# Kernel tuning notes

Measured on AMD Instinct MI355X. Metric: run time of the kernel, lower is better.

Reference implementation:

```python
import jax, jax.numpy as jnp
import numpy as np
import math


def setup_inputs() -> dict:
    key = jax.random.key(0)
    ks = jax.random.split(key, 16)
    B, S, H, K, PREV = 32, 2048, 1024, 4, 2
    sc = 0.02
    return {
        "last_hidden": jax.random.normal(ks[0], (1, B, H), jnp.float32),
        "decoder_inputs": jax.random.normal(ks[1], (B, 1, H), jnp.float32),
        "encoder_outputs": jax.random.normal(ks[2], (B, S, H), jnp.float32),
        "attention_scores": jax.random.normal(ks[3], (PREV, B, 1, S), jnp.float32),
        "attention_mask": jnp.zeros((B, 1, S), jnp.float32),
        "evidence_scores": jax.random.uniform(ks[4], (B,), jnp.float32),
        "evidence_sentence_index": jax.random.randint(ks[5], (B, PREV), 0, S, dtype=jnp.int32),
        "W_ih": jax.random.normal(ks[6], (3 * H, H), jnp.float32) * sc,
        "W_hh": jax.random.normal(ks[7], (3 * H, H), jnp.float32) * sc,
        "b_ih": jax.random.normal(ks[8], (3 * H,), jnp.float32) * sc,
        "b_hh": jax.random.normal(ks[9], (3 * H,), jnp.float32) * sc,
        "Wk": jax.random.normal(ks[10], (H, H), jnp.float32) * sc,
        "bk": jnp.zeros((H,), jnp.float32),
        "Wv": jax.random.normal(ks[11], (H, H), jnp.float32) * sc,
        "bv": jnp.zeros((H,), jnp.float32),
        "topk": K,
    }


def _gru_step(x, h, W_ih, W_hh, b_ih, b_hh):
    # x, h: (B, H). PyTorch GRU cell math.
    gi = x @ W_ih.T + b_ih  # (B, 3H)
    gh = h @ W_hh.T + b_hh  # (B, 3H)
    i_r, i_z, i_n = jnp.split(gi, 3, axis=1)
    h_r, h_z, h_n = jnp.split(gh, 3, axis=1)
    r = jax.nn.sigmoid(i_r + h_r)
    z = jax.nn.sigmoid(i_z + h_z)
    n = jnp.tanh(i_n + r * h_n)
    return (1.0 - z) * n + z * h


def reference(last_hidden, decoder_inputs, encoder_outputs, attention_scores,
              attention_mask, evidence_scores, evidence_sentence_index,
              W_ih, W_hh, b_ih, b_hh, Wk, bk, Wv, bv, topk):
    B, S, H = encoder_outputs.shape
    K = topk
    R = B // K  # real batch (beam groups)

    key_eo = encoder_outputs @ Wk.T + bk    # (B, S, H)
    val_eo = encoder_outputs @ Wv.T + bv    # (B, S, H)

    h_new = _gru_step(decoder_inputs[:, 0], last_hidden[0], W_ih, W_hh, b_ih, b_hh)  # (B, H)
    output = h_new[:, None, :]              # (B, 1, H)

    attn_outputs = jnp.einsum('bih,bsh->bis', output, key_eo) / math.sqrt(H) + attention_mask  # (B,1,S)
    attn_alignment = jax.nn.softmax(attn_outputs, axis=-1)
    context = jnp.einsum('bis,bsh->bih', attn_alignment, val_eo)  # (B, 1, H)

    # top-k per beam, then joint rerank over topk*topk candidates per real example
    vals, idx = jax.lax.top_k(attn_alignment.reshape(R, K, S), K)  # (R, K, K), sorted desc
    scores = vals.reshape(B, K)
    sentences = idx.reshape(B, K)
    log_scores = -jnp.log(scores) + evidence_scores[:, None]       # (B, K)

    flat = log_scores.reshape(R, K * K)
    order = jnp.argsort(flat, axis=-1)[:, :K]                      # (R, K) ascending, stable
    new_evidence_scores = jnp.take_along_axis(flat, order, axis=1).reshape(B)
    s_flat = (order // K + jnp.arange(R)[:, None] * K).reshape(B)  # source beam in [0, B)
    r_flat = (order % K).reshape(B)

    sel_sent = sentences[s_flat, r_flat]                           # (B,)
    result = context[s_flat]                                       # (B, 1, H)
    hidden = h_new[s_flat][None]                                   # (1, B, H)
    new_evidence_sentence_index = jnp.concatenate(
        [evidence_sentence_index[s_flat], sel_sent[:, None].astype(evidence_sentence_index.dtype)], axis=1)
    new_attention_scores = jnp.concatenate(
        [attention_scores[:, s_flat], attn_outputs[s_flat][None]], axis=0)  # (prev+1, B, 1, S)
    new_attention_mask = attention_mask[s_flat]                    # (B, 1, S)

    return (result, hidden, new_evidence_sentence_index,
            new_attention_scores, new_attention_mask, new_evidence_scores)
```

## Files before the change

### kernel.cpp

```cpp
#include <hip/hip_runtime.h>
#include <hip/hip_bf16.h>
#include <cfloat>
#include <climits>
#include <cmath>

#define BB 32
#define SS 2048
#define HH 1024
#define KK 4
#define CH 32

__global__ __launch_bounds__(256) void gates_partial(
    const float* __restrict__ x, const float* __restrict__ h_old,
    const float* __restrict__ W_ih, const float* __restrict__ W_hh,
    float* __restrict__ part) {
  int t = threadIdx.x;
  int jb = blockIdx.x;
  int k0 = blockIdx.y * 64;
  bool second = (jb >= 12);
  const float* A = second ? h_old : x;
  const float* W = second ? W_hh : W_ih;
  int j0 = jb * 256;
  int jr = j0 - (second ? 3072 : 0);
  const float* wp = W + (size_t)(jr + t) * HH + k0;
  float acc[32];
#pragma unroll
  for (int b = 0; b < 32; b++) acc[b] = 0.f;
  for (int kk = 0; kk < 64; kk += 4) {
    float4 wv = *(const float4*)(wp + kk);
#pragma unroll
    for (int b = 0; b < 32; b++) {
      float4 a = *(const float4*)(A + (size_t)b * HH + k0 + kk);
      acc[b] += a.x * wv.x + a.y * wv.y + a.z * wv.z + a.w * wv.w;
    }
  }
  float* pb = part + (size_t)blockIdx.y * (32 * 6144) + j0 + t;
#pragma unroll
  for (int b = 0; b < 32; b++) pb[(size_t)b * 6144] = acc[b];
}

__global__ __launch_bounds__(256) void gru_q(
    const float* __restrict__ part, const float* __restrict__ b_ih,
    const float* __restrict__ b_hh, const float* __restrict__ h_old,
    const float* __restrict__ Wk, float* __restrict__ h_new,
    float* __restrict__ qpart2) {
  __shared__ float hs[256];
  int t = threadIdx.x;
  int kc = blockIdx.x, b = blockIdx.y, z = blockIdx.z;
  int h = kc * 256 + t;
  float s0 = 0.f, s1 = 0.f, s2 = 0.f, s3 = 0.f, s4 = 0.f, s5 = 0.f;
#pragma unroll
  for (int c = 0; c < 16; c++) {
    const float* p = part + ((size_t)c * 32 + b) * 6144;
    s0 += p[h];
    s1 += p[1024 + h];
    s2 += p[2048 + h];
    s3 += p[3072 + h];
    s4 += p[4096 + h];
    s5 += p[5120 + h];
  }
  float ir = s0 + b_ih[h], iz = s1 + b_ih[1024 + h], in_ = s2 + b_ih[2048 + h];
  float hr = s3 + b_hh[h], hz = s4 + b_hh[1024 + h], hn = s5 + b_hh[2048 + h];
  float r = 1.f / (1.f + expf(-(ir + hr)));
  float z_ = 1.f / (1.f + expf(-(iz + hz)));
  float n = tanhf(in_ + r * hn);
  float hv = (1.f - z_) * n + z_ * h_old[b * HH + h];
  if (z == 0) h_new[b * HH + h] = hv;
  hs[t] = hv;
  __syncthreads();
  float2 acc = make_float2(0.f, 0.f);
  const float* wb = Wk + (size_t)kc * 256 * HH + z * 512 + 2 * t;
  for (int k = 0; k < 256; k += 4) {
    float2 w0 = *(const float2*)(wb + (size_t)(k + 0) * HH);
    float2 w1 = *(const float2*)(wb + (size_t)(k + 1) * HH);
    float2 w2 = *(const float2*)(wb + (size_t)(k + 2) * HH);
    float2 w3 = *(const float2*)(wb + (size_t)(k + 3) * HH);
    float a0 = hs[k], a1 = hs[k + 1], a2 = hs[k + 2], a3 = hs[k + 3];
    acc.x += a0 * w0.x + a1 * w1.x + a2 * w2.x + a3 * w3.x;
    acc.y += a0 * w0.y + a1 * w1.y + a2 * w2.y + a3 * w3.y;
  }
  *(float2*)(qpart2 + ((size_t)b * 4 + kc) * HH + z * 512 + 2 * t) = acc;
}

__global__ __launch_bounds__(256) void fused_attn(
    const float* __restrict__ eo, const float* __restrict__ qpart2,
    const float* __restrict__ h_new, const float* __restrict__ bk,
    const float* __restrict__ mask, float* __restrict__ logits,
    float* __restrict__ c0part, float* __restrict__ msum_part) {
  __shared__ float q_lds[HH];
  __shared__ float wred[4];
  __shared__ float cacc[4][1024];
  __shared__ float cms[4][2];
  int b = blockIdx.y, sc = blockIdx.x, t = threadIdx.x;
  int w = t >> 6, lane = t & 63;
  {
    float4 qs = *(const float4*)(qpart2 + ((size_t)b * 4 + 0) * HH + 4 * t);
#pragma unroll
    for (int kc = 1; kc < 4; kc++) {
      float4 v = *(const float4*)(qpart2 + ((size_t)b * 4 + kc) * HH + 4 * t);
      qs.x += v.x; qs.y += v.y; qs.z += v.z; qs.w += v.w;
    }
    *(float4*)&q_lds[4 * t] = qs;
    float4 hv = *(const float4*)(h_new + (size_t)b * HH + 4 * t);
    float4 kv = *(const float4*)(bk + 4 * t);
    float p = hv.x * kv.x + hv.y * kv.y + hv.z * kv.z + hv.w * kv.w;
#pragma unroll
    for (int off = 32; off; off >>= 1) p += __shfl_xor(p, off);
    if (lane == 0) wred[w] = p;
  }
  __syncthreads();
  float hb = wred[0] + wred[1] + wred[2] + wred[3];
  float4 qv[4];
#pragma unroll
  for (int i = 0; i < 4; i++) qv[i] = *(const float4*)&q_lds[(i * 64 + lane) * 4];

  float m = -FLT_MAX, sum = 0.f;
  float4 acc[4];
#pragma unroll
  for (int i = 0; i < 4; i++) acc[i] = make_float4(0.f, 0.f, 0.f, 0.f);
  int rbase = sc * 64 + w * 16;
  for (int tile = 0; tile < 8; tile++) {
    int r0 = rbase + tile * 2;
    float4 rv[2][4];
#pragma unroll
    for (int rr = 0; rr < 2; rr++) {
      const float4* e4 = (const float4*)(eo + ((size_t)b * SS + r0 + rr) * HH);
#pragma unroll
      for (int i = 0; i < 4; i++) rv[rr][i] = e4[i * 64 + lane];
    }
    float p0 = 0.f, p1 = 0.f;
#pragma unroll
    for (int i = 0; i < 4; i++) {
      p0 += rv[0][i].x * qv[i].x + rv[0][i].y * qv[i].y +
            rv[0][i].z * qv[i].z + rv[0][i].w * qv[i].w;
      p1 += rv[1][i].x * qv[i].x + rv[1][i].y * qv[i].y +
            rv[1][i].z * qv[i].z + rv[1][i].w * qv[i].w;
    }
#pragma unroll
    for (int off = 32; off; off >>= 1) {
      p0 += __shfl_xor(p0, off);
      p1 += __shfl_xor(p1, off);
    }
    float lv0 = (p0 + hb) * 0.03125f + mask[(size_t)b * SS + r0];
    float lv1 = (p1 + hb) * 0.03125f + mask[(size_t)b * SS + r0 + 1];
    if (lane == 0) {
      logits[(size_t)b * SS + r0] = lv0;
      logits[(size_t)b * SS + r0 + 1] = lv1;
    }
    float m_new = fmaxf(m, fmaxf(lv0, lv1));
    float scale = expf(m - m_new);
    float w0 = expf(lv0 - m_new), w1 = expf(lv1 - m_new);
    sum = sum * scale + w0 + w1;
#pragma unroll
    for (int i = 0; i < 4; i++) {
      acc[i].x = acc[i].x * scale + w0 * rv[0][i].x + w1 * rv[1][i].x;
      acc[i].y = acc[i].y * scale + w0 * rv[0][i].y + w1 * rv[1][i].y;
      acc[i].z = acc[i].z * scale + w0 * rv[0][i].z + w1 * rv[1][i].z;
      acc[i].w = acc[i].w * scale + w0 * rv[0][i].w + w1 * rv[1][i].w;
    }
    m = m_new;
  }
#pragma unroll
  for (int i = 0; i < 4; i++) *(float4*)&cacc[w][i * 256 + lane * 4] = acc[i];
  if (lane == 0) { cms[w][0] = m; cms[w][1] = sum; }
  __syncthreads();
  float m0 = cms[0][0], m1 = cms[1][0], m2 = cms[2][0], m3 = cms[3][0];
  float mb = fmaxf(fmaxf(m0, m1), fmaxf(m2, m3));
  float wt0 = expf(m0 - mb), wt1 = expf(m1 - mb), wt2 = expf(m2 - mb),
        wt3 = expf(m3 - mb);
  float sb = cms[0][1] * wt0 + cms[1][1] * wt1 + cms[2][1] * wt2 + cms[3][1] * wt3;
  float4 a0 = *(float4*)&cacc[0][4 * t];
  float4 a1 = *(float4*)&cacc[1][4 * t];
  float4 a2 = *(float4*)&cacc[2][4 * t];
  float4 a3 = *(float4*)&cacc[3][4 * t];
  float4 r;
  r.x = wt0 * a0.x + wt1 * a1.x + wt2 * a2.x + wt3 * a3.x;
  r.y = wt0 * a0.y + wt1 * a1.y + wt2 * a2.y + wt3 * a3.y;
  r.z = wt0 * a0.z + wt1 * a1.z + wt2 * a2.z + wt3 * a3.z;
  r.w = wt0 * a0.w + wt1 * a1.w + wt2 * a2.w + wt3 * a3.w;
  *(float4*)(c0part + ((size_t)sc * 32 + b) * 1024 + 4 * t) = r;
  if (t == 0) {
    msum_part[((size_t)sc * 32 + b) * 2 + 0] = mb;
    msum_part[((size_t)sc * 32 + b) * 2 + 1] = sb;
  }
}

__device__ __forceinline__ bool vi_better(float av, int ai, float bv, int bi) {
  return av > bv || (av == bv && ai < bi);
}

__global__ __launch_bounds__(256) void attn_finish(
    const float* __restrict__ c0part, const float* __restrict__ msum_part,
    const float* __restrict__ logits, float* __restrict__ c0,
    float* __restrict__ scores, int* __restrict__ sent) {
  int bid = blockIdx.x, t = threadIdx.x;
  int b = (bid < 128) ? (bid >> 2) : (bid - 128);
  float m = -FLT_MAX;
  float ms[CH];
#pragma unroll
  for (int c = 0; c < CH; c++) {
    ms[c] = msum_part[((size_t)c * 32 + b) * 2 + 0];
    m = fmaxf(m, ms[c]);
  }
  float sum = 0.f;
  float wc[CH];
#pragma unroll
  for (int c = 0; c < CH; c++) {
    wc[c] = expf(ms[c] - m);
    sum += msum_part[((size_t)c * 32 + b) * 2 + 1] * wc[c];
  }
  float inv = 1.f / sum;

  if (bid < 128) {
    int h = (bid & 3) * 256 + t;
    float a = 0.f;
#pragma unroll
    for (int c = 0; c < CH; c++)
      a += wc[c] * c0part[((size_t)c * 32 + b) * 1024 + h];
    c0[(size_t)b * HH + h] = a * inv;
    return;
  }

  float tv0 = -FLT_MAX, tv1 = -FLT_MAX, tv2 = -FLT_MAX, tv3 = -FLT_MAX;
  int ti0 = INT_MAX, ti1 = INT_MAX, ti2 = INT_MAX, ti3 = INT_MAX;
#pragma unroll
  for (int it = 0; it < 8; it++) {
    int idx = it * 256 + t;
    float v = logits[(size_t)b * SS + idx];
    if (vi_better(v, idx, tv3, ti3)) {
      tv3 = v; ti3 = idx;
      if (vi_better(tv3, ti3, tv2, ti2)) { float fv = tv2; int fi = ti2; tv2 = tv3; ti2 = ti3; tv3 = fv; ti3 = fi; }
      if (vi_better(tv2, ti2, tv1, ti1)) { float fv = tv1; int fi = ti1; tv1 = tv2; ti1 = ti2; tv2 = fv; ti2 = fi; }
      if (vi_better(tv1, ti1, tv0, ti0)) { float fv = tv0; int fi = ti0; tv0 = tv1; ti0 = ti1; tv1 = fv; ti1 = fi; }
    }
  }
  __shared__ float sv[256][4];
  __shared__ int si[256][4];
  sv[t][0] = tv0; sv[t][1] = tv1; sv[t][2] = tv2; sv[t][3] = tv3;
  si[t][0] = ti0; si[t][1] = ti1; si[t][2] = ti2; si[t][3] = ti3;
  __syncthreads();
  for (int off = 128; off; off >>= 1) {
    if (t < off) {
      float bv0 = sv[t + off][0], bv1 = sv[t + off][1], bv2 = sv[t + off][2], bv3 = sv[t + off][3];
      int bi0 = si[t + off][0], bi1 = si[t + off][1], bi2 = si[t + off][2], bi3 = si[t + off][3];
      float mv0, mv1, mv2, mv3; int mi0, mi1, mi2, mi3;
      if (vi_better(tv0, ti0, bv3, bi3)) { mv0 = tv0; mi0 = ti0; } else { mv0 = bv3; mi0 = bi3; }
      if (vi_better(tv1, ti1, bv2, bi2)) { mv1 = tv1; mi1 = ti1; } else { mv1 = bv2; mi1 = bi2; }
      if (vi_better(tv2, ti2, bv1, bi1)) { mv2 = tv2; mi2 = ti2; } else { mv2 = bv1; mi2 = bi1; }
      if (vi_better(tv3, ti3, bv0, bi0)) { mv3 = tv3; mi3 = ti3; } else { mv3 = bv0; mi3 = bi0; }
      if (!vi_better(mv0, mi0, mv2, mi2)) { float fv = mv0; int fi = mi0; mv0 = mv2; mi0 = mi2; mv2 = fv; mi2 = fi; }
      if (!vi_better(mv1, mi1, mv3, mi3)) { float fv = mv1; int fi = mi1; mv1 = mv3; mi1 = mi3; mv3 = fv; mi3 = fi; }
      if (!vi_better(mv0, mi0, mv1, mi1)) { float fv = mv0; int fi = mi0; mv0 = mv1; mi0 = mi1; mv1 = fv; mi1 = fi; }
      if (!vi_better(mv2, mi2, mv3, mi3)) { float fv = mv2; int fi = mi2; mv2 = mv3; mi2 = mi3; mv3 = fv; mi3 = fi; }
      tv0 = mv0; tv1 = mv1; tv2 = mv2; tv3 = mv3;
      ti0 = mi0; ti1 = mi1; ti2 = mi2; ti3 = mi3;
      sv[t][0] = tv0; sv[t][1] = tv1; sv[t][2] = tv2; sv[t][3] = tv3;
      si[t][0] = ti0; si[t][1] = ti1; si[t][2] = ti2; si[t][3] = ti3;
    }
    __syncthreads();
  }
  if (t == 0) {
    scores[b * KK + 0] = expf(tv0 - m) * inv; sent[b * KK + 0] = ti0;
    scores[b * KK + 1] = expf(tv1 - m) * inv; sent[b * KK + 1] = ti1;
    scores[b * KK + 2] = expf(tv2 - m) * inv; sent[b * KK + 2] = ti2;
    scores[b * KK + 3] = expf(tv3 - m) * inv; sent[b * KK + 3] = ti3;
  }
}

__global__ __launch_bounds__(256) void ctx_sel_gather(
    const float* __restrict__ scores, const int* __restrict__ sent,
    const float* __restrict__ evidence, const int* __restrict__ esi,
    const float* __restrict__ Wv, const float* __restrict__ bvec,
    const float* __restrict__ c0, const float* __restrict__ hnew,
    const float* __restrict__ attn_in, const float* __restrict__ logits,
    const float* __restrict__ mask, float* __restrict__ out0,
    float* __restrict__ out1, float* __restrict__ out2,
    float* __restrict__ out3, float* __restrict__ out4,
    float* __restrict__ out5) {
  __shared__ int s_sh;
  __shared__ float cs[HH];
  int jq = blockIdx.x, b = blockIdx.y, t = threadIdx.x;
  if (t == 0) {
    int r = b >> 2, j = b & 3;
    float ls[16];
    bool used[16];
    for (int k1 = 0; k1 < 4; k1++)
      for (int k2 = 0; k2 < 4; k2++)
        ls[k1 * 4 + k2] = -logf(scores[(r * 4 + k1) * 4 + k2]) + evidence[r * 4 + k1];
    for (int i = 0; i < 16; i++) used[i] = false;
    int best = 0;
    float bvv = FLT_MAX;
    for (int jj = 0; jj <= j; jj++) {
      best = 0;
      bvv = FLT_MAX;
      for (int i = 0; i < 16; i++)
        if (!used[i] && ls[i] < bvv) { bvv = ls[i]; best = i; }
      used[best] = true;
    }
    int k1 = best >> 2, k2 = best & 3;
    int sSel = r * 4 + k1;
    s_sh = sSel;
    if (jq == 0) {
      out5[b] = bvv;
      out2[b * 3 + 0] = (float)esi[sSel * 2 + 0];
      out2[b * 3 + 1] = (float)esi[sSel * 2 + 1];
      out2[b * 3 + 2] = (float)sent[sSel * 4 + k2];
    }
  }
  __syncthreads();
  int s = s_sh;
  *(float4*)&cs[4 * t] = *(const float4*)(c0 + (size_t)s * HH + 4 * t);
  __syncthreads();
  {
    int j = jq * 256 + t;
    const float4* w4 = (const float4*)(Wv + (size_t)j * HH);
    float acc = bvec[j];
#pragma unroll 8
    for (int k4 = 0; k4 < 256; k4++) {
      float4 wv = w4[k4];
      float4 cc = *(const float4*)&cs[4 * k4];
      acc += wv.x * cc.x + wv.y * cc.y + wv.z * cc.z + wv.w * cc.w;
    }
    out0[(size_t)b * HH + j] = acc;
  }
  out1[(size_t)b * HH + jq * 256 + t] = hnew[(size_t)s * HH + jq * 256 + t];
#pragma unroll
  for (int p = 0; p < 2; p++) {
    *(float2*)(out3 + ((size_t)p * BB + b) * SS + jq * 512 + 2 * t) =
        *(const float2*)(attn_in + ((size_t)p * BB + s) * SS + jq * 512 + 2 * t);
  }
  *(float2*)(out3 + ((size_t)2 * BB + b) * SS + jq * 512 + 2 * t) =
      *(const float2*)(logits + (size_t)s * SS + jq * 512 + 2 * t);
  *(float2*)(out4 + (size_t)b * SS + jq * 512 + 2 * t) =
      *(const float2*)(mask + (size_t)s * SS + jq * 512 + 2 * t);
}

extern "C" void kernel_launch(void* const* d_in, const int* in_sizes, int n_in,
                              void* d_out, int out_size, void* d_ws, size_t ws_size,
                              hipStream_t stream) {
  const float* h_old = (const float*)d_in[0];
  const float* x     = (const float*)d_in[1];
  const float* eo    = (const float*)d_in[2];
  const float* attn_in = (const float*)d_in[3];
  const float* mask  = (const float*)d_in[4];
  const float* evidence = (const float*)d_in[5];
  const int*   esi   = (const int*)d_in[6];
  const float* W_ih  = (const float*)d_in[7];
  const float* W_hh  = (const float*)d_in[8];
  const float* b_ih  = (const float*)d_in[9];
  const float* b_hh  = (const float*)d_in[10];
  const float* Wk    = (const float*)d_in[11];
  const float* bk    = (const float*)d_in[12];
  const float* Wv    = (const float*)d_in[13];
  const float* bv    = (const float*)d_in[14];

  float* w = (float*)d_ws;
  float* h_new  = w + 0;
  float* logits = w + 32768;
  float* scores = w + 98304;
  int*   sent   = (int*)(w + 98432);
  float* c0     = w + 98560;
  float* msum_part = w + 131328;
  float* c0part = w + 133376;
  float* gpart  = w + 1181952;
  float* qpart2 = w + 4327680;

  float* out0 = (float*)d_out;
  float* out1 = out0 + 32768;
  float* out2 = out1 + 32768;
  float* out3 = out2 + 96;
  float* out4 = out3 + 196608;
  float* out5 = out4 + 65536;

  gates_partial<<<dim3(24, 16), 256, 0, stream>>>(x, h_old, W_ih, W_hh, gpart);
  gru_q<<<dim3(4, 32, 2), 256, 0, stream>>>(gpart, b_ih, b_hh, h_old, Wk, h_new, qpart2);
  fused_attn<<<dim3(CH, BB), 256, 0, stream>>>(eo, qpart2, h_new, bk, mask,
                                               logits, c0part, msum_part);
  attn_finish<<<160, 256, 0, stream>>>(c0part, msum_part, logits, c0, scores, sent);
  ctx_sel_gather<<<dim3(4, BB), 256, 0, stream>>>(
      scores, sent, evidence, esi, Wv, bv, c0, h_new, attn_in, logits, mask,
      out0, out1, out2, out3, out4, out5);
}
```

Baseline: 135.3 us.

## Split GRU gate GEMV across batch groups and separate Wk projection into partial+reduce

The gate GEMV grid gains a batch-quarter dimension, so each block accumulates 8 batch rows instead of 32, giving four times more blocks and fewer registers per thread. The fused GRU+Wk kernel is split into a pointwise GRU kernel plus a Wk projection kernel that is partitioned over 32-row chunks of the reduction dimension and batch groups, followed by a separate reduction kernel. This is meant to raise parallelism and occupancy for the small-batch matrix-vector work. In exchange it adds two kernel launches and re-reads the weight matrices once per batch group.

```diff
diff --git a/kernel.cpp b/kernel.cpp
--- a/kernel.cpp
+++ b/kernel.cpp
@@ -16,38 +16,39 @@
     float* __restrict__ part) {
   int t = threadIdx.x;
   int jb = blockIdx.x;
-  int k0 = blockIdx.y * 64;
+  int kc = blockIdx.y;
+  int bq = blockIdx.z;
+  int k0 = kc * 64;
   bool second = (jb >= 12);
-  const float* A = second ? h_old : x;
+  const float* A = (second ? h_old : x) + (size_t)(bq * 8) * HH;
   const float* W = second ? W_hh : W_ih;
   int j0 = jb * 256;
   int jr = j0 - (second ? 3072 : 0);
   const float* wp = W + (size_t)(jr + t) * HH + k0;
-  float acc[32];
-#pragma unroll
-  for (int b = 0; b < 32; b++) acc[b] = 0.f;
+  float acc[8];
+#pragma unroll
+  for (int bi = 0; bi < 8; bi++) acc[bi] = 0.f;
+#pragma unroll
   for (int kk = 0; kk < 64; kk += 4) {
     float4 wv = *(const float4*)(wp + kk);
 #pragma unroll
-    for (int b = 0; b < 32; b++) {
-      float4 a = *(const float4*)(A + (size_t)b * HH + k0 + kk);
-      acc[b] += a.x * wv.x + a.y * wv.y + a.z * wv.z + a.w * wv.w;
-    }
-  }
-  float* pb = part + (size_t)blockIdx.y * (32 * 6144) + j0 + t;
-#pragma unroll
-  for (int b = 0; b < 32; b++) pb[(size_t)b * 6144] = acc[b];
-}
-
-__global__ __launch_bounds__(256) void gru_q(
+    for (int bi = 0; bi < 8; bi++) {
+      float4 a = *(const float4*)(A + (size_t)bi * HH + k0 + kk);
+      acc[bi] += a.x * wv.x + a.y * wv.y + a.z * wv.z + a.w * wv.w;
+    }
+  }
+  float* pb = part + ((size_t)kc * 32 + bq * 8) * 6144 + j0 + t;
+#pragma unroll
+  for (int bi = 0; bi < 8; bi++) pb[(size_t)bi * 6144] = acc[bi];
+}
+
+__global__ __launch_bounds__(256) void gru_pw(
     const float* __restrict__ part, const float* __restrict__ b_ih,
     const float* __restrict__ b_hh, const float* __restrict__ h_old,
-    const float* __restrict__ Wk, float* __restrict__ h_new,
-    float* __restrict__ qpart2) {
-  __shared__ float hs[256];
+    float* __restrict__ h_new) {
   int t = threadIdx.x;
-  int kc = blockIdx.x, b = blockIdx.y, z = blockIdx.z;
-  int h = kc * 256 + t;
+  int b = blockIdx.x;
+  int h = blockIdx.y * 256 + t;
   float s0 = 0.f, s1 = 0.f, s2 = 0.f, s3 = 0.f, s4 = 0.f, s5 = 0.f;
 #pragma unroll
   for (int c = 0; c < 16; c++) {
@@ -62,28 +63,51 @@
   float ir = s0 + b_ih[h], iz = s1 + b_ih[1024 + h], in_ = s2 + b_ih[2048 + h];
   float hr = s3 + b_hh[h], hz = s4 + b_hh[1024 + h], hn = s5 + b_hh[2048 + h];
   float r = 1.f / (1.f + expf(-(ir + hr)));
-  float z_ = 1.f / (1.f + expf(-(iz + hz)));
+  float z = 1.f / (1.f + expf(-(iz + hz)));
   float n = tanhf(in_ + r * hn);
-  float hv = (1.f - z_) * n + z_ * h_old[b * HH + h];
-  if (z == 0) h_new[b * HH + h] = hv;
-  hs[t] = hv;
-  __syncthreads();
-  float2 acc = make_float2(0.f, 0.f);
-  const float* wb = Wk + (size_t)kc * 256 * HH + z * 512 + 2 * t;
-  for (int k = 0; k < 256; k += 4) {
-    float2 w0 = *(const float2*)(wb + (size_t)(k + 0) * HH);
-    float2 w1 = *(const float2*)(wb + (size_t)(k + 1) * HH);
-    float2 w2 = *(const float2*)(wb + (size_t)(k + 2) * HH);
-    float2 w3 = *(const float2*)(wb + (size_t)(k + 3) * HH);
-    float a0 = hs[k], a1 = hs[k + 1], a2 = hs[k + 2], a3 = hs[k + 3];
-    acc.x += a0 * w0.x + a1 * w1.x + a2 * w2.x + a3 * w3.x;
-    acc.y += a0 * w0.y + a1 * w1.y + a2 * w2.y + a3 * w3.y;
-  }
-  *(float2*)(qpart2 + ((size_t)b * 4 + kc) * HH + z * 512 + 2 * t) = acc;
+  h_new[b * HH + h] = (1.f - z) * n + z * h_old[b * HH + h];
+}
+
+__global__ __launch_bounds__(256) void q_partial(const float* __restrict__ hnew,
+                                                 const float* __restrict__ Wk,
+                                                 float* __restrict__ qpart) {
+  int t = threadIdx.x;
+  int n = blockIdx.x * 256 + t;
+  int j0 = blockIdx.y * 32;
+  int b0 = blockIdx.z * 8;
+  float acc[8];
+#pragma unroll
+  for (int bi = 0; bi < 8; bi++) acc[bi] = 0.f;
+#pragma unroll
+  for (int j = 0; j < 32; j += 4) {
+    float w0 = Wk[(size_t)(j0 + j + 0) * HH + n];
+    float w1 = Wk[(size_t)(j0 + j + 1) * HH + n];
+    float w2 = Wk[(size_t)(j0 + j + 2) * HH + n];
+    float w3 = Wk[(size_t)(j0 + j + 3) * HH + n];
+#pragma unroll
+    for (int bi = 0; bi < 8; bi++) {
+      float4 hv = *(const float4*)(hnew + (size_t)(b0 + bi) * HH + j0 + j);
+      acc[bi] += hv.x * w0 + hv.y * w1 + hv.z * w2 + hv.w * w3;
+    }
+  }
+  float* pb = qpart + ((size_t)blockIdx.y * 32 + b0) * 1024 + n;
+#pragma unroll
+  for (int bi = 0; bi < 8; bi++) pb[(size_t)bi * 1024] = acc[bi];
+}
+
+__global__ __launch_bounds__(256) void q_reduce(const float* __restrict__ qpart,
+                                                float* __restrict__ q) {
+  int t = threadIdx.x;
+  int b = blockIdx.x >> 2;
+  int n = (blockIdx.x & 3) * 256 + t;
+  float s = 0.f;
+#pragma unroll
+  for (int jc = 0; jc < 32; jc++) s += qpart[((size_t)jc * 32 + b) * 1024 + n];
+  q[b * HH + n] = s;
 }
 
 __global__ __launch_bounds__(256) void fused_attn(
-    const float* __restrict__ eo, const float* __restrict__ qpart2,
+    const float* __restrict__ eo, const float* __restrict__ q,
     const float* __restrict__ h_new, const float* __restrict__ bk,
     const float* __restrict__ mask, float* __restrict__ logits,
     float* __restrict__ c0part, float* __restrict__ msum_part) {
@@ -94,12 +118,7 @@
   int b = blockIdx.y, sc = blockIdx.x, t = threadIdx.x;
   int w = t >> 6, lane = t & 63;
   {
-    float4 qs = *(const float4*)(qpart2 + ((size_t)b * 4 + 0) * HH + 4 * t);
-#pragma unroll
-    for (int kc = 1; kc < 4; kc++) {
-      float4 v = *(const float4*)(qpart2 + ((size_t)b * 4 + kc) * HH + 4 * t);
-      qs.x += v.x; qs.y += v.y; qs.z += v.z; qs.w += v.w;
-    }
+    float4 qs = *(const float4*)(q + (size_t)b * HH + 4 * t);
     *(float4*)&q_lds[4 * t] = qs;
     float4 hv = *(const float4*)(h_new + (size_t)b * HH + 4 * t);
     float4 kv = *(const float4*)(bk + 4 * t);
@@ -356,14 +375,15 @@
 
   float* w = (float*)d_ws;
   float* h_new  = w + 0;
-  float* logits = w + 32768;
-  float* scores = w + 98304;
-  int*   sent   = (int*)(w + 98432);
-  float* c0     = w + 98560;
-  float* msum_part = w + 131328;
-  float* c0part = w + 133376;
-  float* gpart  = w + 1181952;
-  float* qpart2 = w + 4327680;
+  float* q      = w + 32768;
+  float* logits = w + 65536;
+  float* scores = w + 131072;
+  int*   sent   = (int*)(w + 131200);
+  float* c0     = w + 131328;
+  float* msum_part = w + 164096;
+  float* c0part = w + 166144;
+  float* gpart  = w + 1214720;
+  float* qpart  = w + 4360448;
 
   float* out0 = (float*)d_out;
   float* out1 = out0 + 32768;
@@ -372,10 +392,12 @@
   float* out4 = out3 + 196608;
   float* out5 = out4 + 65536;
 
-  gates_partial<<<dim3(24, 16), 256, 0, stream>>>(x, h_old, W_ih, W_hh, gpart);
-  gru_q<<<dim3(4, 32, 2), 256, 0, stream>>>(gpart, b_ih, b_hh, h_old, Wk, h_new, qpart2);
-  fused_attn<<<dim3(CH, BB), 256, 0, stream>>>(eo, qpart2, h_new, bk, mask,
-                                               logits, c0part, msum_part);
+  gates_partial<<<dim3(24, 16, 4), 256, 0, stream>>>(x, h_old, W_ih, W_hh, gpart);
+  gru_pw<<<dim3(32, 4), 256, 0, stream>>>(gpart, b_ih, b_hh, h_old, h_new);
+  q_partial<<<dim3(4, 32, 4), 256, 0, stream>>>(h_new, Wk, qpart);
+  q_reduce<<<128, 256, 0, stream>>>(qpart, q);
+  fused_attn<<<dim3(CH, BB), 256, 0, stream>>>(eo, q, h_new, bk, mask, logits,
+                                               c0part, msum_part);
   attn_finish<<<160, 256, 0, stream>>>(c0part, msum_part, logits, c0, scores, sent);
   ctx_sel_gather<<<dim3(4, BB), 256, 0, stream>>>(
       scores, sent, evidence, esi, Wv, bv, c0, h_new, attn_in, logits, mask,
```

Measured after the change: 127.5 us, median of 2. -5.8%, faster.
